# Performance work log

Hardware: AMD Instinct MI355X
Metric: run time of the kernel (lower is better)

The kernel has to match this reference:

```python
import jax, jax.numpy as jnp
import numpy as np

GROUP_SIZE = 128  # K-rows sharing one dequant scale


def _dequant(B, s):
    """Unpack int4 (uint4b8: value = nibble - 8) from packed int32 and apply group scales.
    B: [K//8, N] int32, 8 nibbles per word along K (nibble i -> k = 8*row + i).
    s: [K//GROUP_SIZE, N] float scales.
    Returns W: [K, N] float.
    """
    Kp, N = B.shape
    K = Kp * 8
    shifts = (jnp.arange(8, dtype=jnp.int32) * 4)
    # [Kp, 8, N] nibbles -> [K, N]
    nib = (B[:, None, :] >> shifts[None, :, None]) & 0xF
    w = nib.reshape(K, N).astype(s.dtype) - 8.0
    # per-group scaling: groups of GROUP_SIZE consecutive K rows
    w = (w.reshape(K // GROUP_SIZE, GROUP_SIZE, N) * s[:, None, :]).reshape(K, N)
    return w


def setup_inputs() -> dict:
    key = jax.random.key(0)
    k1, k2, k3 = jax.random.split(key, 3)
    M, K, N = 64, 8192, 8192
    x = jax.random.normal(k1, (M, K), dtype=jnp.float32)
    B = jax.random.randint(k2, (K // 8, N), 0, 2147483647, dtype=jnp.int32)
    s = jax.random.uniform(k3, (K // GROUP_SIZE, N), dtype=jnp.float32) * 0.02
    return {"x": x, "B": B, "s": s}


def reference(x, B, s):
    # machete_mm: fused int4 dequant + GEMM; here expressed as dequant then matmul
    w = _dequant(B, s)          # [K, N]
    out = x @ w                 # [M, N]
    return out
```

## Files before the change

kernel.cpp:

```cpp
#include <hip/hip_runtime.h>

typedef _Float16 half2v __attribute__((ext_vector_type(2)));
typedef _Float16 half8  __attribute__((ext_vector_type(8)));
typedef float    floatx4 __attribute__((ext_vector_type(4)));

#define M_DIM 64
#define K_DIM 8192
#define N_DIM 8192
#define NT 512
#define KSB 16

__global__ __launch_bounds__(256) void permute_x_kernel(
        const float* __restrict__ x, _Float16* __restrict__ xp) {
    const int t  = blockIdx.x * 256 + threadIdx.x;
    const int c  = t & 15;
    const int q  = (t >> 4) & 3;
    const int mt = (t >> 6) & 3;
    const int kb = t >> 8;
    const int m  = mt * 16 + c;
    const int k0 = kb * 32 + q * 8;
    const float* src = x + (size_t)m * K_DIM + k0;
    float4 a = *(const float4*)(src);
    float4 b = *(const float4*)(src + 4);
    union { _Float16 h[8]; float4 f; } u;
    u.h[0] = (_Float16)a.x; u.h[1] = (_Float16)b.x;
    u.h[2] = (_Float16)a.y; u.h[3] = (_Float16)b.y;
    u.h[4] = (_Float16)a.z; u.h[5] = (_Float16)b.z;
    u.h[6] = (_Float16)a.w; u.h[7] = (_Float16)b.w;
    *(float4*)(xp + (size_t)t * 8) = u.f;
}

__device__ __forceinline__ void dma16(const void* g, void* l) {
    __builtin_amdgcn_global_load_lds(
        (const __attribute__((address_space(1))) unsigned int*)(uintptr_t)g,
        (__attribute__((address_space(3))) unsigned int*)(uintptr_t)l,
        16, 0, 0);
}

__device__ __forceinline__ half2v dq_pair(unsigned int bits, half2v sub, half2v sc) {
    union { unsigned int u; half2v h; } cv;
    cv.u = bits;
    return (cv.h - sub) * sc;
}

__global__ __launch_bounds__(1024, 4) void machete_mm_kernel(
        const _Float16* __restrict__ xp,
        const unsigned int* __restrict__ Bq,
        const float* __restrict__ s,
        _Float16* __restrict__ partial) {
    __shared__ char astage[2][16384];

    const int tid  = threadIdx.x;
    const int w    = tid >> 6;
    const int lane = tid & 63;
    const int c    = lane & 15;
    const int q    = lane >> 4;
    const int ns   = blockIdx.x;
    const int kb   = blockIdx.y;
    const int wc   = ns * NT + w * 32;

    half2v s2[4][2];
    #pragma unroll
    for (int g = 0; g < 4; ++g) {
        const float f0 = s[(size_t)(kb * 4 + g) * N_DIM + wc + c];
        const float f1 = s[(size_t)(kb * 4 + g) * N_DIM + wc + 16 + c];
        s2[g][0] = (half2v){ (_Float16)f0, (_Float16)f0 };
        s2[g][1] = (half2v){ (_Float16)f1, (_Float16)f1 };
    }
    const half2v c1032 = { (_Float16)1032.0f, (_Float16)1032.0f };

    const char* a_base = (const char*)xp + (size_t)kb * 65536;
    const unsigned int* b_base = Bq + (size_t)(kb * 64) * N_DIM + wc + c;

    auto bload = [&](int st, int d, int t) {
        return b_base[(size_t)(st * 16 + d * 4 + q) * N_DIM + 16 * t];
    };
    auto stage_dma = [&](int st, int p) {
        dma16(a_base + (size_t)st * 16384 + w * 1024 + lane * 16,
              &astage[p][w * 1024]);
    };

    floatx4 acc[4][2];
    #pragma unroll
    for (int i = 0; i < 4; ++i) { acc[i][0] = (floatx4)0.0f; acc[i][1] = (floatx4)0.0f; }

    unsigned int bcur[2][4], bnxt[2][4];
    #pragma unroll
    for (int d = 0; d < 4; ++d) { bcur[0][d] = bload(0, d, 0); bcur[1][d] = bload(0, d, 1); }
    stage_dma(0, 0);
    __syncthreads();

    #pragma unroll
    for (int st = 0; st < 4; ++st) {
        const int p = st & 1;
        if (st < 3) {
            #pragma unroll
            for (int d = 0; d < 4; ++d) {
                bnxt[0][d] = bload(st + 1, d, 0);
                bnxt[1][d] = bload(st + 1, d, 1);
            }
            stage_dma(st + 1, p ^ 1);
        }

        #pragma unroll
        for (int d = 0; d < 4; ++d) {
            half8 afr[4];
            #pragma unroll
            for (int mt = 0; mt < 4; ++mt)
                afr[mt] = *(const half8*)(&astage[p][(d * 4 + mt) * 1024 + lane * 16]);
            #pragma unroll
            for (int t = 0; t < 2; ++t) {
                const unsigned int wd = bcur[t][d];
                const half2v sc = s2[st][t];
                union { half2v h2[4]; half8 h8; } b8;
                b8.h2[0] = dq_pair(( wd        & 0x000F000Fu) | 0x64006400u, c1032, sc);
                b8.h2[1] = dq_pair(((wd >> 4)  & 0x000F000Fu) | 0x64006400u, c1032, sc);
                b8.h2[2] = dq_pair(((wd >> 8)  & 0x000F000Fu) | 0x64006400u, c1032, sc);
                b8.h2[3] = dq_pair(((wd >> 12) & 0x000F000Fu) | 0x64006400u, c1032, sc);
                #pragma unroll
                for (int mt = 0; mt < 4; ++mt)
                    acc[mt][t] = __builtin_amdgcn_mfma_f32_16x16x32_f16(
                        afr[mt], b8.h8, acc[mt][t], 0, 0, 0);
            }
        }
        __syncthreads();
        #pragma unroll
        for (int d = 0; d < 4; ++d) { bcur[0][d] = bnxt[0][d]; bcur[1][d] = bnxt[1][d]; }
    }

    _Float16* pt = partial + (size_t)(kb * M_DIM) * N_DIM;
    #pragma unroll
    for (int mt = 0; mt < 4; ++mt)
        #pragma unroll
        for (int t = 0; t < 2; ++t)
            #pragma unroll
            for (int r = 0; r < 4; ++r) {
                const int m = mt * 16 + q * 4 + r;
                pt[(size_t)m * N_DIM + wc + 16 * t + c] = (_Float16)acc[mt][t][r];
            }
}

__global__ __launch_bounds__(256) void reduce_kernel(
        const _Float16* __restrict__ partial, float* __restrict__ out) {
    const size_t i = ((size_t)blockIdx.x * 256 + threadIdx.x) * 8;
    const size_t S = (size_t)M_DIM * N_DIM;
    float a[8] = {0, 0, 0, 0, 0, 0, 0, 0};
    #pragma unroll
    for (int bk = 0; bk < KSB; ++bk) {
        const half8 hv = *(const half8*)(partial + bk * S + i);
        #pragma unroll
        for (int j = 0; j < 8; ++j) a[j] += (float)hv[j];
    }
    float4 v0 = { a[0], a[1], a[2], a[3] };
    float4 v1 = { a[4], a[5], a[6], a[7] };
    *(float4*)(out + i)     = v0;
    *(float4*)(out + i + 4) = v1;
}

extern "C" void kernel_launch(void* const* d_in, const int* in_sizes, int n_in,
                              void* d_out, int out_size, void* d_ws, size_t ws_size,
                              hipStream_t stream) {
    const float*        x  = (const float*)d_in[0];
    const unsigned int* Bq = (const unsigned int*)d_in[1];
    const float*        sc = (const float*)d_in[2];
    float* out        = (float*)d_out;
    _Float16* xp      = (_Float16*)d_ws;
    _Float16* partial = (_Float16*)((char*)d_ws + (1 << 20));

    permute_x_kernel<<<dim3(M_DIM * K_DIM / 8 / 256), 256, 0, stream>>>(x, xp);
    machete_mm_kernel<<<dim3(N_DIM / NT, KSB), 1024, 0, stream>>>(xp, Bq, sc, partial);
    reduce_kernel<<<dim3(M_DIM * N_DIM / (256 * 8)), 256, 0, stream>>>(partial, out);
}
```

Before: 96.05 us.

## Halve block size and give each wave 64 output columns for A-fragment reuse

Each block now runs 8 waves instead of 16, and each wave computes four 16-column N tiles instead of two, so every A fragment read from LDS feeds twice as many MFMAs. Each wave issues two DMA copies per stage to fill the same A staging buffer. Scale loads move from kernel entry into each stage to limit register pressure. Accumulators and prefetched B words per thread double, which raises VGPR use and may lower occupancy or cause spills.

```diff
diff --git a/kernel.cpp b/kernel.cpp
--- a/kernel.cpp
+++ b/kernel.cpp
@@ -43,7 +43,7 @@
     return (cv.h - sub) * sc;
 }
 
-__global__ __launch_bounds__(1024, 4) void machete_mm_kernel(
+__global__ __launch_bounds__(512, 4) void machete_mm_kernel(
         const _Float16* __restrict__ xp,
         const unsigned int* __restrict__ Bq,
         const float* __restrict__ s,
@@ -57,48 +57,56 @@
     const int q    = lane >> 4;
     const int ns   = blockIdx.x;
     const int kb   = blockIdx.y;
-    const int wc   = ns * NT + w * 32;
+    const int wc   = ns * NT + w * 64;
 
-    half2v s2[4][2];
-    #pragma unroll
-    for (int g = 0; g < 4; ++g) {
-        const float f0 = s[(size_t)(kb * 4 + g) * N_DIM + wc + c];
-        const float f1 = s[(size_t)(kb * 4 + g) * N_DIM + wc + 16 + c];
-        s2[g][0] = (half2v){ (_Float16)f0, (_Float16)f0 };
-        s2[g][1] = (half2v){ (_Float16)f1, (_Float16)f1 };
-    }
     const half2v c1032 = { (_Float16)1032.0f, (_Float16)1032.0f };
 
     const char* a_base = (const char*)xp + (size_t)kb * 65536;
     const unsigned int* b_base = Bq + (size_t)(kb * 64) * N_DIM + wc + c;
+    const float*        s_base = s + (size_t)(kb * 4) * N_DIM + wc + c;
 
     auto bload = [&](int st, int d, int t) {
         return b_base[(size_t)(st * 16 + d * 4 + q) * N_DIM + 16 * t];
     };
     auto stage_dma = [&](int st, int p) {
-        dma16(a_base + (size_t)st * 16384 + w * 1024 + lane * 16,
-              &astage[p][w * 1024]);
+        #pragma unroll
+        for (int k = 0; k < 2; ++k) {
+            const int idx = k * 8 + w;
+            dma16(a_base + (size_t)st * 16384 + idx * 1024 + lane * 16,
+                  &astage[p][idx * 1024]);
+        }
     };
 
-    floatx4 acc[4][2];
+    floatx4 acc[4][4];
     #pragma unroll
-    for (int i = 0; i < 4; ++i) { acc[i][0] = (floatx4)0.0f; acc[i][1] = (floatx4)0.0f; }
+    for (int i = 0; i < 4; ++i)
+        #pragma unroll
+        for (int j = 0; j < 4; ++j) acc[i][j] = (floatx4)0.0f;
 
-    unsigned int bcur[2][4], bnxt[2][4];
+    unsigned int bcur[4][4], bnxt[4][4];
     #pragma unroll
-    for (int d = 0; d < 4; ++d) { bcur[0][d] = bload(0, d, 0); bcur[1][d] = bload(0, d, 1); }
+    for (int d = 0; d < 4; ++d)
+        #pragma unroll
+        for (int t = 0; t < 4; ++t) bcur[t][d] = bload(0, d, t);
     stage_dma(0, 0);
     __syncthreads();
 
     #pragma unroll
     for (int st = 0; st < 4; ++st) {
         const int p = st & 1;
+
+        half2v s2[4];
+        #pragma unroll
+        for (int t = 0; t < 4; ++t) {
+            const float f = s_base[(size_t)st * N_DIM + 16 * t];
+            s2[t] = (half2v){ (_Float16)f, (_Float16)f };
+        }
+
         if (st < 3) {
             #pragma unroll
-            for (int d = 0; d < 4; ++d) {
-                bnxt[0][d] = bload(st + 1, d, 0);
-                bnxt[1][d] = bload(st + 1, d, 1);
-            }
+            for (int d = 0; d < 4; ++d)
+                #pragma unroll
+                for (int t = 0; t < 4; ++t) bnxt[t][d] = bload(st + 1, d, t);
             stage_dma(st + 1, p ^ 1);
         }
 
@@ -109,9 +117,9 @@
             for (int mt = 0; mt < 4; ++mt)
                 afr[mt] = *(const half8*)(&astage[p][(d * 4 + mt) * 1024 + lane * 16]);
             #pragma unroll
-            for (int t = 0; t < 2; ++t) {
+            for (int t = 0; t < 4; ++t) {
                 const unsigned int wd = bcur[t][d];
-                const half2v sc = s2[st][t];
+                const half2v sc = s2[t];
                 union { half2v h2[4]; half8 h8; } b8;
                 b8.h2[0] = dq_pair(( wd        & 0x000F000Fu) | 0x64006400u, c1032, sc);
                 b8.h2[1] = dq_pair(((wd >> 4)  & 0x000F000Fu) | 0x64006400u, c1032, sc);
@@ -124,15 +132,19 @@
             }
         }
         __syncthreads();
-        #pragma unroll
-        for (int d = 0; d < 4; ++d) { bcur[0][d] = bnxt[0][d]; bcur[1][d] = bnxt[1][d]; }
+        if (st < 3) {
+            #pragma unroll
+            for (int d = 0; d < 4; ++d)
+                #pragma unroll
+                for (int t = 0; t < 4; ++t) bcur[t][d] = bnxt[t][d];
+        }
     }
 
     _Float16* pt = partial + (size_t)(kb * M_DIM) * N_DIM;
     #pragma unroll
     for (int mt = 0; mt < 4; ++mt)
         #pragma unroll
-        for (int t = 0; t < 2; ++t)
+        for (int t = 0; t < 4; ++t)
             #pragma unroll
             for (int r = 0; r < 4; ++r) {
                 const int m = mt * 16 + q * 4 + r;
@@ -168,6 +180,6 @@
     _Float16* partial = (_Float16*)((char*)d_ws + (1 << 20));
 
     permute_x_kernel<<<dim3(M_DIM * K_DIM / 8 / 256), 256, 0, stream>>>(x, xp);
-    machete_mm_kernel<<<dim3(N_DIM / NT, KSB), 1024, 0, stream>>>(xp, Bq, sc, partial);
+    machete_mm_kernel<<<dim3(N_DIM / NT, KSB), 512, 0, stream>>>(xp, Bq, sc, partial);
     reduce_kernel<<<dim3(M_DIM * N_DIM / (256 * 8)), 256, 0, stream>>>(partial, out);
 }
```

After: 97.65 us. Within noise of the previous version (+1.7%).

## Stage B tiles via async global-to-LDS DMA and coalesce partial stores through LDS

Applied to the files above, without the earlier changes.

Packed int4 B tiles are now loaded with global_load_lds DMA into padded LDS buffers, double-buffered alongside the A stage, rather than into registers with scattered 4-byte loads. The epilogue writes accumulators into an LDS scratch tile and then emits 16-byte row-contiguous stores of the fp16 partial sums. This aims to cut poorly coalesced global traffic on both B reads and partial writes. In exchange it uses more LDS, which can limit occupancy, and adds extra barriers in the epilogue.

```diff
diff --git a/kernel.cpp b/kernel.cpp
--- a/kernel.cpp
+++ b/kernel.cpp
@@ -9,6 +9,8 @@
 #define N_DIM 8192
 #define NT 512
 #define KSB 16
+#define BSTRIDE 516
+#define EPSTRIDE 520
 
 __global__ __launch_bounds__(256) void permute_x_kernel(
         const float* __restrict__ x, _Float16* __restrict__ xp) {
@@ -48,7 +50,10 @@
         const unsigned int* __restrict__ Bq,
         const float* __restrict__ s,
         _Float16* __restrict__ partial) {
-    __shared__ char astage[2][16384];
+    __shared__ char lds[32768 + 2 * BSTRIDE * 16 * 4];
+    char*         ablk  = lds;
+    unsigned int* bblk  = (unsigned int*)(lds + 32768);
+    _Float16*     ep    = (_Float16*)(lds + 32768);
 
     const int tid  = threadIdx.x;
     const int w    = tid >> 6;
@@ -59,6 +64,8 @@
     const int kb   = blockIdx.y;
     const int wc   = ns * NT + w * 32;
 
+    const half2v c1032 = { (_Float16)1032.0f, (_Float16)1032.0f };
+
     half2v s2[4][2];
     #pragma unroll
     for (int g = 0; g < 4; ++g) {
@@ -67,50 +74,41 @@
         s2[g][0] = (half2v){ (_Float16)f0, (_Float16)f0 };
         s2[g][1] = (half2v){ (_Float16)f1, (_Float16)f1 };
     }
-    const half2v c1032 = { (_Float16)1032.0f, (_Float16)1032.0f };
 
     const char* a_base = (const char*)xp + (size_t)kb * 65536;
-    const unsigned int* b_base = Bq + (size_t)(kb * 64) * N_DIM + wc + c;
+    const char* b_base = (const char*)Bq;
 
-    auto bload = [&](int st, int d, int t) {
-        return b_base[(size_t)(st * 16 + d * 4 + q) * N_DIM + 16 * t];
-    };
     auto stage_dma = [&](int st, int p) {
         dma16(a_base + (size_t)st * 16384 + w * 1024 + lane * 16,
-              &astage[p][w * 1024]);
+              ablk + p * 16384 + w * 1024);
+        const size_t brow = (size_t)(kb * 64 + st * 16 + w) * N_DIM + ns * NT;
+        unsigned int* bdst = bblk + p * (BSTRIDE * 16) + w * BSTRIDE;
+        dma16(b_base + brow * 4 +        lane * 16, bdst);
+        dma16(b_base + brow * 4 + 1024 + lane * 16, bdst + 256);
     };
 
     floatx4 acc[4][2];
     #pragma unroll
     for (int i = 0; i < 4; ++i) { acc[i][0] = (floatx4)0.0f; acc[i][1] = (floatx4)0.0f; }
 
-    unsigned int bcur[2][4], bnxt[2][4];
-    #pragma unroll
-    for (int d = 0; d < 4; ++d) { bcur[0][d] = bload(0, d, 0); bcur[1][d] = bload(0, d, 1); }
     stage_dma(0, 0);
     __syncthreads();
 
     #pragma unroll
     for (int st = 0; st < 4; ++st) {
         const int p = st & 1;
-        if (st < 3) {
-            #pragma unroll
-            for (int d = 0; d < 4; ++d) {
-                bnxt[0][d] = bload(st + 1, d, 0);
-                bnxt[1][d] = bload(st + 1, d, 1);
-            }
-            stage_dma(st + 1, p ^ 1);
-        }
+        if (st < 3) stage_dma(st + 1, p ^ 1);
 
+        const unsigned int* bs = bblk + p * (BSTRIDE * 16);
         #pragma unroll
         for (int d = 0; d < 4; ++d) {
             half8 afr[4];
             #pragma unroll
             for (int mt = 0; mt < 4; ++mt)
-                afr[mt] = *(const half8*)(&astage[p][(d * 4 + mt) * 1024 + lane * 16]);
+                afr[mt] = *(const half8*)(ablk + p * 16384 + (d * 4 + mt) * 1024 + lane * 16);
             #pragma unroll
             for (int t = 0; t < 2; ++t) {
-                const unsigned int wd = bcur[t][d];
+                const unsigned int wd = bs[(d * 4 + q) * BSTRIDE + w * 32 + 16 * t + c];
                 const half2v sc = s2[st][t];
                 union { half2v h2[4]; half8 h8; } b8;
                 b8.h2[0] = dq_pair(( wd        & 0x000F000Fu) | 0x64006400u, c1032, sc);
@@ -124,20 +122,33 @@
             }
         }
         __syncthreads();
-        #pragma unroll
-        for (int d = 0; d < 4; ++d) { bcur[0][d] = bnxt[0][d]; bcur[1][d] = bnxt[1][d]; }
     }
 
-    _Float16* pt = partial + (size_t)(kb * M_DIM) * N_DIM;
+    _Float16* pt = partial + (size_t)(kb * M_DIM) * N_DIM + ns * NT;
     #pragma unroll
-    for (int mt = 0; mt < 4; ++mt)
+    for (int r = 0; r < 2; ++r) {
+        if (r) __syncthreads();
         #pragma unroll
-        for (int t = 0; t < 2; ++t)
+        for (int h = 0; h < 2; ++h) {
+            const int mt = 2 * r + h;
+            const int ml = h * 16 + q * 4;
             #pragma unroll
-            for (int r = 0; r < 4; ++r) {
-                const int m = mt * 16 + q * 4 + r;
-                pt[(size_t)m * N_DIM + wc + 16 * t + c] = (_Float16)acc[mt][t][r];
-            }
+            for (int t = 0; t < 2; ++t)
+                #pragma unroll
+                for (int rr = 0; rr < 4; ++rr)
+                    ep[(ml + rr) * EPSTRIDE + w * 32 + 16 * t + c] =
+                        (_Float16)acc[mt][t][rr];
+        }
+        __syncthreads();
+        const int row = tid >> 5;
+        const int seg = tid & 31;
+        const _Float16* src = ep + row * EPSTRIDE + seg * 16;
+        uint4 u0 = *(const uint4*)(src);
+        uint4 u1 = *(const uint4*)(src + 8);
+        _Float16* dst = pt + (size_t)(r * 32 + row) * N_DIM + seg * 16;
+        *(uint4*)(dst)     = u0;
+        *(uint4*)(dst + 8) = u1;
+    }
 }
 
 __global__ __launch_bounds__(256) void reduce_kernel(
```

Result: no change. 96.21 us (+0.2%).

## Fuse split-K reduction into GEMM via last-block atomic counter, halve N tile

Applied to the files above, without the earlier changes.

The separate reduce kernel is removed. Each GEMM block now bumps a per-strip atomic counter after writing its fp16 partials, and the last of the KSB blocks for a strip sums all partials and writes the fp32 output. The N strip shrinks from 512 to 256 columns with 512-thread blocks, which doubles the grid, and each thread now issues two A-tile DMAs. This saves a kernel launch and lets the reduction overlap with other blocks, at the cost of threadfence and atomic overhead and a serialized tail where only one block per strip does the reduce.

```diff
diff --git a/kernel.cpp b/kernel.cpp
--- a/kernel.cpp
+++ b/kernel.cpp
@@ -7,11 +7,14 @@
 #define M_DIM 64
 #define K_DIM 8192
 #define N_DIM 8192
-#define NT 512
+#define NT 256
+#define NSTRIPS (N_DIM / NT)
 #define KSB 16
 
 __global__ __launch_bounds__(256) void permute_x_kernel(
-        const float* __restrict__ x, _Float16* __restrict__ xp) {
+        const float* __restrict__ x, _Float16* __restrict__ xp,
+        int* __restrict__ cnt) {
+    if (blockIdx.x == 0 && threadIdx.x < NSTRIPS) cnt[threadIdx.x] = 0;
     const int t  = blockIdx.x * 256 + threadIdx.x;
     const int c  = t & 15;
     const int q  = (t >> 4) & 3;
@@ -43,12 +46,15 @@
     return (cv.h - sub) * sc;
 }
 
-__global__ __launch_bounds__(1024, 4) void machete_mm_kernel(
+__global__ __launch_bounds__(512, 4) void machete_mm_kernel(
         const _Float16* __restrict__ xp,
         const unsigned int* __restrict__ Bq,
         const float* __restrict__ s,
-        _Float16* __restrict__ partial) {
-    __shared__ char astage[2][16384];
+        _Float16* __restrict__ partial,
+        int* __restrict__ cnt,
+        float* __restrict__ out) {
+    __shared__ char ablk[2][16384];
+    __shared__ int  sflag;
 
     const int tid  = threadIdx.x;
     const int w    = tid >> 6;
@@ -59,6 +65,8 @@
     const int kb   = blockIdx.y;
     const int wc   = ns * NT + w * 32;
 
+    const half2v c1032 = { (_Float16)1032.0f, (_Float16)1032.0f };
+
     half2v s2[4][2];
     #pragma unroll
     for (int g = 0; g < 4; ++g) {
@@ -67,7 +75,6 @@
         s2[g][0] = (half2v){ (_Float16)f0, (_Float16)f0 };
         s2[g][1] = (half2v){ (_Float16)f1, (_Float16)f1 };
     }
-    const half2v c1032 = { (_Float16)1032.0f, (_Float16)1032.0f };
 
     const char* a_base = (const char*)xp + (size_t)kb * 65536;
     const unsigned int* b_base = Bq + (size_t)(kb * 64) * N_DIM + wc + c;
@@ -76,8 +83,12 @@
         return b_base[(size_t)(st * 16 + d * 4 + q) * N_DIM + 16 * t];
     };
     auto stage_dma = [&](int st, int p) {
-        dma16(a_base + (size_t)st * 16384 + w * 1024 + lane * 16,
-              &astage[p][w * 1024]);
+        #pragma unroll
+        for (int k = 0; k < 2; ++k) {
+            const int idx = k * 8 + w;
+            dma16(a_base + (size_t)st * 16384 + idx * 1024 + lane * 16,
+                  &ablk[p][idx * 1024]);
+        }
     };
 
     floatx4 acc[4][2];
@@ -107,7 +118,7 @@
             half8 afr[4];
             #pragma unroll
             for (int mt = 0; mt < 4; ++mt)
-                afr[mt] = *(const half8*)(&astage[p][(d * 4 + mt) * 1024 + lane * 16]);
+                afr[mt] = *(const half8*)(&ablk[p][(d * 4 + mt) * 1024 + lane * 16]);
             #pragma unroll
             for (int t = 0; t < 2; ++t) {
                 const unsigned int wd = bcur[t][d];
@@ -124,8 +135,10 @@
             }
         }
         __syncthreads();
-        #pragma unroll
-        for (int d = 0; d < 4; ++d) { bcur[0][d] = bnxt[0][d]; bcur[1][d] = bnxt[1][d]; }
+        if (st < 3) {
+            #pragma unroll
+            for (int d = 0; d < 4; ++d) { bcur[0][d] = bnxt[0][d]; bcur[1][d] = bnxt[1][d]; }
+        }
     }
 
     _Float16* pt = partial + (size_t)(kb * M_DIM) * N_DIM;
@@ -138,23 +151,31 @@
                 const int m = mt * 16 + q * 4 + r;
                 pt[(size_t)m * N_DIM + wc + 16 * t + c] = (_Float16)acc[mt][t][r];
             }
-}
 
-__global__ __launch_bounds__(256) void reduce_kernel(
-        const _Float16* __restrict__ partial, float* __restrict__ out) {
-    const size_t i = ((size_t)blockIdx.x * 256 + threadIdx.x) * 8;
-    const size_t S = (size_t)M_DIM * N_DIM;
-    float a[8] = {0, 0, 0, 0, 0, 0, 0, 0};
-    #pragma unroll
-    for (int bk = 0; bk < KSB; ++bk) {
-        const half8 hv = *(const half8*)(partial + bk * S + i);
+    __threadfence();
+    if (tid == 0) sflag = atomicAdd(&cnt[ns], 1);
+    __syncthreads();
+    if (sflag == KSB - 1) {
+        __threadfence();
+        const size_t S = (size_t)M_DIM * N_DIM;
         #pragma unroll
-        for (int j = 0; j < 8; ++j) a[j] += (float)hv[j];
+        for (int task = 0; task < 4; ++task) {
+            const int idx = task * 512 + tid;
+            const int m   = idx >> 5;
+            const int cg  = idx & 31;
+            const size_t off = (size_t)m * N_DIM + ns * NT + cg * 8;
+            float a[8] = {0, 0, 0, 0, 0, 0, 0, 0};
+            for (int bk = 0; bk < KSB; ++bk) {
+                const half8 hv = *(const half8*)(partial + bk * S + off);
+                #pragma unroll
+                for (int j = 0; j < 8; ++j) a[j] += (float)hv[j];
+            }
+            float4 v0 = { a[0], a[1], a[2], a[3] };
+            float4 v1 = { a[4], a[5], a[6], a[7] };
+            *(float4*)(out + off)     = v0;
+            *(float4*)(out + off + 4) = v1;
+        }
     }
-    float4 v0 = { a[0], a[1], a[2], a[3] };
-    float4 v1 = { a[4], a[5], a[6], a[7] };
-    *(float4*)(out + i)     = v0;
-    *(float4*)(out + i + 4) = v1;
 }
 
 extern "C" void kernel_launch(void* const* d_in, const int* in_sizes, int n_in,
@@ -166,8 +187,8 @@
     float* out        = (float*)d_out;
     _Float16* xp      = (_Float16*)d_ws;
     _Float16* partial = (_Float16*)((char*)d_ws + (1 << 20));
+    int*      cnt     = (int*)((char*)d_ws + (17 << 20));
 
-    permute_x_kernel<<<dim3(M_DIM * K_DIM / 8 / 256), 256, 0, stream>>>(x, xp);
-    machete_mm_kernel<<<dim3(N_DIM / NT, KSB), 1024, 0, stream>>>(xp, Bq, sc, partial);
-    reduce_kernel<<<dim3(M_DIM * N_DIM / (256 * 8)), 256, 0, stream>>>(partial, out);
+    permute_x_kernel<<<dim3(M_DIM * K_DIM / 8 / 256), 256, 0, stream>>>(x, xp, cnt);
+    machete_mm_kernel<<<dim3(NSTRIPS, KSB), 512, 0, stream>>>(xp, Bq, sc, partial, cnt, out);
 }
```

After: 237.8 us. 2.48x slower.
